# Kernel optimization log

Hardware: AMD Instinct MI355X
Metric: run time of the kernel (lower is better)

Reference implementation:

```python
import jax, jax.numpy as jnp
import numpy as np

N = 100000   # node_count
F = 128      # dim_in (also top-k pool size: k = ceil(F/N * N) = F)
E = 625000   # edges


def setup_inputs() -> dict:
    key = jax.random.key(0)
    ks = jax.random.split(key, 20)
    s = 1.0 / np.sqrt(F)

    def g(i, shape, scale=s):
        return jax.random.normal(ks[i], shape, dtype=jnp.float32) * scale

    inp = {
        "x": jax.random.normal(ks[0], (N, F), dtype=jnp.float32),
        "edge_index": jax.random.randint(ks[1], (2, E), 0, N),
        "edge_weight": jax.random.uniform(ks[2], (E,), dtype=jnp.float32),
    }
    for l in (1, 2):
        b = 3 + 6 * (l - 1)
        inp[f"p{l}"] = g(b, (F,))              # TopKPooling projection vector
        inp[f"w_ih{l}"] = g(b + 1, (3 * F, F))  # GRU input weights (r,z,n)
        inp[f"w_hh{l}"] = g(b + 2, (3 * F, F))  # GRU hidden weights
        inp[f"b_ih{l}"] = g(b + 3, (3 * F,))
        inp[f"b_hh{l}"] = g(b + 4, (3 * F,))
        inp[f"h0{l}"] = g(b + 5, (F, F))        # EvolveGCNH initial_weight
    inp["lin1_w"] = g(15, (2, F))
    inp["lin1_b"] = g(16, (2,), 0.1)
    inp["lin2_w"] = g(17, (1, 2), 0.5)
    inp["lin2_b"] = g(18, (1,), 0.1)
    return inp


def _gru_step(x_t, h, w_ih, w_hh, b_ih, b_hh):
    # single GRU timestep, batch = F rows, hidden = F
    gi = x_t @ w_ih.T + b_ih
    gh = h @ w_hh.T + b_hh
    i_r, i_z, i_n = jnp.split(gi, 3, axis=-1)
    h_r, h_z, h_n = jnp.split(gh, 3, axis=-1)
    r = jax.nn.sigmoid(i_r + h_r)
    z = jax.nn.sigmoid(i_z + h_z)
    n = jnp.tanh(i_n + r * h_n)
    return (1.0 - z) * n + z * h


def _gcn_conv_fixed_w(x, W, edge_index, edge_weight):
    # GCN with externally supplied weight: out = D^-1/2 (A+I) D^-1/2 (x W)
    row, col = edge_index[0], edge_index[1]
    loops = jnp.arange(N)
    row = jnp.concatenate([row, loops])
    col = jnp.concatenate([col, loops])
    w = jnp.concatenate([edge_weight, jnp.ones((N,), x.dtype)])
    deg = jax.ops.segment_sum(w, col, num_segments=N)
    dinv = jnp.where(deg > 0, jax.lax.rsqrt(deg), 0.0)
    norm = dinv[row] * w * dinv[col]          # [E+N]
    xw = x @ W                                 # [N, F]
    return jax.ops.segment_sum(norm[:, None] * xw[row], col, num_segments=N)


def _evolve_gcnh(x, edge_index, edge_weight, p, w_ih, w_hh, b_ih, b_hh, h0):
    # TopKPooling: score = x@p / ||p||, keep top F nodes, gate by tanh(score)
    score = x @ p / jnp.linalg.norm(p)
    top_vals, top_idx = jax.lax.top_k(score, F)
    x_tilde = x[top_idx] * jnp.tanh(top_vals)[:, None]   # [F, F]
    # evolve weight via one GRU step (hidden = previous/initial weight)
    W = _gru_step(x_tilde, h0, w_ih, w_hh, b_ih, b_hh)   # [F, F]
    return _gcn_conv_fixed_w(x, W, edge_index, edge_weight)


def reference(x, edge_index, edge_weight,
              p1, w_ih1, w_hh1, b_ih1, b_hh1, h01,
              p2, w_ih2, w_hh2, b_ih2, b_hh2, h02,
              lin1_w, lin1_b, lin2_w, lin2_b):
    h = jax.nn.relu(_evolve_gcnh(x, edge_index, edge_weight, p1, w_ih1, w_hh1, b_ih1, b_hh1, h01))
    h = jax.nn.relu(_evolve_gcnh(h, edge_index, edge_weight, p2, w_ih2, w_hh2, b_ih2, b_hh2, h02))
    # dropout(0.4) is identity in eval mode
    h = h @ lin1_w.T + lin1_b
    h = h @ lin2_w.T + lin2_b
    return h  # [N, 1]
```

## Files before the change

kernel.cpp:

```cpp
#include <hip/hip_runtime.h>
#include <cstdint>
#include <cstddef>


#define FDIM 128

typedef __attribute__((ext_vector_type(8))) short bfrag;
typedef __attribute__((ext_vector_type(4))) float f32x4;
typedef __attribute__((ext_vector_type(2))) float f32x2;

__device__ __forceinline__ float wave_sum(float v) {
#pragma unroll
  for (int m = 32; m >= 1; m >>= 1) v += __shfl_xor(v, m, 64);
  return v;
}

__device__ __forceinline__ float sigmoidf_(float x) {
  return 1.0f / (1.0f + expf(-x));
}

__device__ __forceinline__ unsigned omap(float f) {
  unsigned u = __float_as_uint(f);
  return (u & 0x80000000u) ? ~u : (u | 0x80000000u);
}

__device__ __forceinline__ int xcd_chunk(int b, int nb) {
  return (b & 7) * (nb >> 3) + (b >> 3);
}

__device__ __forceinline__ int swz(int row, int colb) {
  return row * 256 + (colb ^ ((row & 7) << 4));
}


__global__ __launch_bounds__(256) void k_edge_samp(
    const int* __restrict__ ei, const float* __restrict__ ew,
    float* deg, int* cnt, int E,
    const float* __restrict__ x, const float* __restrict__ p1,
    float* __restrict__ samp, int stride, int eb) {
  if ((int)blockIdx.x < eb) {
    int e = blockIdx.x * 256 + threadIdx.x;
    if (e < E) {
      int c = ei[E + e];
      atomicAdd(&deg[c], ew[e]);
      atomicAdd(&cnt[c], 1);
    }
  } else {
    int l = threadIdx.x & 63;
    int w = ((int)blockIdx.x - eb) * 4 + ((int)threadIdx.x >> 6);
    float2 pv = ((const float2*)p1)[l];
    float inv = 1.0f / sqrtf(wave_sum(pv.x * pv.x + pv.y * pv.y));
#pragma unroll
    for (int r = 0; r < 4; r++) {
      int si = w * 4 + r;
      float2 a = ((const float2*)(x + (size_t)(si * stride) * FDIM))[l];
      float s = wave_sum(a.x * pv.x + a.y * pv.y) * inv;
      if (l == 0) samp[si] = s;
    }
  }
}


__global__ __launch_bounds__(256) void k_scan1_thr(
    const int* __restrict__ cnt, int* bsum,
    const float* __restrict__ deg, float* __restrict__ dinv, int n, int nb,
    const float* __restrict__ samp, float* __restrict__ thr) {
  __shared__ float a[2048];
  int t = threadIdx.x;
  if ((int)blockIdx.x < nb) {
    int* s = (int*)a;
    int b = blockIdx.x;
    int base = b * 1024;
    int v = 0;
#pragma unroll
    for (int j = 0; j < 4; j++) {
      int i = base + j * 256 + t;
      if (i < n) { v += cnt[i]; dinv[i] = 1.0f / sqrtf(1.0f + deg[i]); }
    }
    s[t] = v; __syncthreads();
    for (int off = 128; off > 0; off >>= 1) {
      if (t < off) s[t] += s[t + off];
      __syncthreads();
    }
    if (t == 0) bsum[b] = s[0];
  } else {
    for (int i = t; i < 2048; i += 256) a[i] = samp[i];
    __syncthreads();
    int g = ((int)blockIdx.x - nb) * 256 + t;
    int j = g >> 2, sub = g & 3;
    float v = a[j];
    int gt = 0, eq = 0;
    const float4* a4 = (const float4*)(a + sub * 512);
#pragma unroll 8
    for (int i = 0; i < 128; i++) {
      float4 b4 = a4[i];
      gt += (b4.x > v) + (b4.y > v) + (b4.z > v) + (b4.w > v);
      eq += (b4.x == v) + (b4.y == v) + (b4.z == v) + (b4.w == v);
    }
    gt += __shfl_xor(gt, 1, 64); eq += __shfl_xor(eq, 1, 64);
    gt += __shfl_xor(gt, 2, 64); eq += __shfl_xor(eq, 2, 64);
    if (sub == 0 && gt <= 15 && gt + eq > 15) thr[0] = v;
  }
}


__global__ __launch_bounds__(1024) void k_scan23(const int* __restrict__ cnt,
                                                 const int* __restrict__ bsum,
                                                 int* rstart, int* rnext,
                                                 int n, int nb, int E_) {
  __shared__ int s[1024];
  __shared__ int bs[128];
  int b = blockIdx.x, t = threadIdx.x;
  if (t < nb) bs[t] = bsum[t];
  __syncthreads();
  if (t == 0) {
    int run = 0;
    for (int k = 0; k < nb; k++) { int v = bs[k]; bs[k] = run; run += v; }
  }
  __syncthreads();
  int base = bs[b];
  int i = b * 1024 + t;
  int v = (i < n) ? cnt[i] : 0;
  s[t] = v; __syncthreads();
  for (int off = 1; off < 1024; off <<= 1) {
    int tmp = (t >= off) ? s[t - off] : 0;
    __syncthreads();
    s[t] += tmp;
    __syncthreads();
  }
  if (i < n) { int ex = base + s[t] - v; rstart[i] = ex; rnext[i] = ex; }
  if (b == 0 && t == 0) rstart[n] = E_;
}

__global__ void k_fill(const int* __restrict__ ei, const float* __restrict__ ew,
                       const float* __restrict__ dinv, int* rnext, int2* pay, int E) {
  int e = blockIdx.x * blockDim.x + threadIdx.x;
  if (e < E) {
    int r = ei[e];
    int c = ei[E + e];
    float nm = dinv[r] * ew[e] * dinv[c];
    int pos = atomicAdd(&rnext[c], 1);
    pay[pos] = make_int2(r, __float_as_int(nm));
  }
}


__global__ __launch_bounds__(256) void k_thr16s(const float* __restrict__ src, int stride,
                                                float* __restrict__ thr) {
  __shared__ float a[2048];
  int t = threadIdx.x;
  for (int i = t; i < 2048; i += 256) a[i] = src[(size_t)i * stride];
  __syncthreads();
  int g = blockIdx.x * 256 + t;
  int j = g >> 2, sub = g & 3;
  float v = a[j];
  int gt = 0, eq = 0;
  const float4* a4 = (const float4*)(a + sub * 512);
#pragma unroll 8
  for (int i = 0; i < 128; i++) {
    float4 b = a4[i];
    gt += (b.x > v) + (b.y > v) + (b.z > v) + (b.w > v);
    eq += (b.x == v) + (b.y == v) + (b.z == v) + (b.w == v);
  }
  gt += __shfl_xor(gt, 1, 64); eq += __shfl_xor(eq, 1, 64);
  gt += __shfl_xor(gt, 2, 64); eq += __shfl_xor(eq, 2, 64);
  if (sub == 0 && gt <= 15 && gt + eq > 15) thr[0] = v;
}

__global__ void k_collect(const float* __restrict__ sc, const float* __restrict__ thr,
                          unsigned long long* candk, int* csel, int n) {
  int i = blockIdx.x * blockDim.x + threadIdx.x;
  if (i >= n) return;
  float s = sc[i];
  if (s >= thr[0]) {
    int pos = atomicAdd(csel, 1);
    if (pos < 4096)
      candk[pos] = ((unsigned long long)omap(s) << 32) | (unsigned)(~(unsigned)i);
  }
}

__global__ __launch_bounds__(1024) void k_sel(const unsigned long long* __restrict__ candk,
                                              const int* __restrict__ csel,
                                              int* tidx, float* ttanh) {
  __shared__ unsigned long long a[4104];
  int t = threadIdx.x;
  int nc = csel[0]; if (nc > 4096) nc = 4096;
  int ncp = (nc + 7) & ~7;
  for (int i = t; i < ncp; i += 1024) a[i] = (i < nc) ? candk[i] : 0ULL;
  __syncthreads();
  for (int j = t; j < nc; j += 1024) {
    unsigned long long key = a[j];
    int r = 0;
#pragma unroll 8
    for (int i = 0; i < ncp; i++) r += (a[i] > key);
    if (r < 128) {
      unsigned idx = ~(unsigned)key;
      unsigned hi = (unsigned)(key >> 32);
      unsigned u = (hi & 0x80000000u) ? (hi ^ 0x80000000u) : ~hi;
      tidx[r] = (int)idx;
      ttanh[r] = tanhf(__uint_as_float(u));
    }
  }
}


template <int BF16IN>
__global__ __launch_bounds__(384) void k_gru(const void* __restrict__ xinv,
                                             const int* __restrict__ tidx,
                                             const float* __restrict__ ttanh,
                                             const float* __restrict__ wih,
                                             const float* __restrict__ whh,
                                             const float* __restrict__ bih,
                                             const float* __restrict__ bhh,
                                             const float* __restrict__ h0,
                                             unsigned short* __restrict__ WT_hi,
                                             unsigned short* __restrict__ WT_lo) {
  __shared__ float xt[128], hs[128], gis[384], ghs[384];
  int r = blockIdx.x, t = threadIdx.x;
  if (t < 128) {
    int idx = tidx[r];
    float xv;
    if (BF16IN) {
      unsigned short u = ((const unsigned short*)xinv)[(size_t)idx * FDIM + t];
      xv = __uint_as_float((unsigned)u << 16);
    } else {
      xv = ((const float*)xinv)[(size_t)idx * FDIM + t];
    }
    xt[t] = xv * ttanh[r];
    hs[t] = h0[r * FDIM + t];
  }
  __syncthreads();
  float gi = bih[t], gh = bhh[t];
  const float4* wi4 = (const float4*)(wih + (size_t)t * FDIM);
  const float4* wh4 = (const float4*)(whh + (size_t)t * FDIM);
#pragma unroll 8
  for (int k = 0; k < 32; k++) {
    float4 av = wi4[k], bv = wh4[k];
    gi += av.x * xt[4 * k] + av.y * xt[4 * k + 1] + av.z * xt[4 * k + 2] + av.w * xt[4 * k + 3];
    gh += bv.x * hs[4 * k] + bv.y * hs[4 * k + 1] + bv.z * hs[4 * k + 2] + bv.w * hs[4 * k + 3];
  }
  gis[t] = gi; ghs[t] = gh;
  __syncthreads();
  if (t < 128) {
    float rg = sigmoidf_(gis[t] + ghs[t]);
    float zg = sigmoidf_(gis[t + 128] + ghs[t + 128]);
    float ng = tanhf(gis[t + 256] + rg * ghs[t + 256]);
    float w = (1.0f - zg) * ng + zg * hs[t];
    unsigned u = __float_as_uint(w);
    float res = w - __uint_as_float(u & 0xFFFF0000u);
    WT_hi[t * FDIM + r] = (unsigned short)(u >> 16);
    WT_lo[t * FDIM + r] = (unsigned short)(__float_as_uint(res) >> 16);
  }
}


template <int MODE>
__global__ __launch_bounds__(256) void k_gemm5(const float* __restrict__ Af,
                                               const unsigned short* __restrict__ Ab,
                                               const unsigned short* __restrict__ BTh,
                                               const unsigned short* __restrict__ BTl,
                                               unsigned short* __restrict__ Y2,
                                               float* __restrict__ scOut,
                                               const float* __restrict__ p2,
                                               const float* __restrict__ l1w,
                                               const float* __restrict__ l1b,
                                               const float* __restrict__ l2w,
                                               const float* __restrict__ l2b,
                                               int nrows) {
  __shared__ unsigned short sBh[128 * 128];
  __shared__ unsigned short sBl[128 * 128];
  int tid = threadIdx.x;
  int eb = xcd_chunk(blockIdx.x, gridDim.x);
  int rblk = eb * 128;
  if (rblk >= nrows) return;
  for (int i = tid; i < 2048; i += 256) {
    int row = i >> 4, colb = (i & 15) << 4;
    *(uint4*)((char*)sBh + swz(row, colb)) = ((const uint4*)BTh)[i];
    *(uint4*)((char*)sBl + swz(row, colb)) = ((const uint4*)BTl)[i];
  }
  __syncthreads();
  int wv = tid >> 6, l = tid & 63;
  int lcol = l & 15;
  int kgrp = (l >> 4) * 8;

  float pv[8];
  float scale;
  if (MODE == 1) {
#pragma unroll
    for (int ct = 0; ct < 8; ct++) pv[ct] = p2[ct * 16 + lcol];
    float lp = 0.f;
#pragma unroll
    for (int ct = 0; ct < 8; ct++) lp += pv[ct] * pv[ct];
#pragma unroll
    for (int m = 1; m < 16; m <<= 1) lp += __shfl_xor(lp, m, 64);
    scale = 1.0f / sqrtf(lp);
  } else {
    float w0 = l2w[0], w1 = l2w[1];
#pragma unroll
    for (int ct = 0; ct < 8; ct++)
      pv[ct] = w0 * l1w[ct * 16 + lcol] + w1 * l1w[128 + ct * 16 + lcol];
    scale = w0 * l1b[0] + w1 * l1b[1] + l2b[0];
  }

  for (int tile = 0; tile < 2; tile++) {
    int r0 = rblk + wv * 32 + tile * 16;
    if (r0 >= nrows) break;
    int arow = min(r0 + lcol, nrows - 1);
    f32x4 acc[8];
#pragma unroll
    for (int c = 0; c < 8; c++) acc[c] = (f32x4){0.f, 0.f, 0.f, 0.f};
#pragma unroll
    for (int ks = 0; ks < 4; ks++) {
      bfrag ah, al;
      if (MODE == 1) {
        const float* xp = Af + (size_t)arow * FDIM + kgrp + ks * 32;
        float4 v0 = *(const float4*)(xp);
        float4 v1 = *(const float4*)(xp + 4);
        float xs[8] = {v0.x, v0.y, v0.z, v0.w, v1.x, v1.y, v1.z, v1.w};
#pragma unroll
        for (int i = 0; i < 8; i++) {
          unsigned u = __float_as_uint(xs[i]);
          float res = xs[i] - __uint_as_float(u & 0xFFFF0000u);
          ah[i] = (short)(u >> 16);
          al[i] = (short)(__float_as_uint(res) >> 16);
        }
      } else {
        ah = *(const bfrag*)(Ab + (size_t)arow * FDIM + kgrp + ks * 32);
      }
      int colb = (ks * 32 + kgrp) * 2;
#pragma unroll
      for (int ct = 0; ct < 8; ct++) {
        int off = swz(ct * 16 + lcol, colb);
        bfrag bh = *(const bfrag*)((const char*)sBh + off);
        bfrag bl = *(const bfrag*)((const char*)sBl + off);
        acc[ct] = __builtin_amdgcn_mfma_f32_16x16x32_bf16(ah, bh, acc[ct], 0, 0, 0);
        acc[ct] = __builtin_amdgcn_mfma_f32_16x16x32_bf16(ah, bl, acc[ct], 0, 0, 0);
        if (MODE == 1)
          acc[ct] = __builtin_amdgcn_mfma_f32_16x16x32_bf16(al, bh, acc[ct], 0, 0, 0);
      }
    }
    int rbase = r0 + (l >> 4) * 4;
    float part[4] = {0.f, 0.f, 0.f, 0.f};
#pragma unroll
    for (int ct = 0; ct < 8; ct++) {
      int col = ct * 16 + lcol;
#pragma unroll
      for (int r = 0; r < 4; r++) {
        int row = rbase + r;
        float rl = fmaxf(acc[ct][r], 0.0f);
        part[r] += rl * pv[ct];
        if (MODE == 1 && row < nrows) {
          unsigned u = __float_as_uint(rl);
          Y2[(size_t)row * FDIM + col] = (unsigned short)((u + 0x8000u) >> 16);
        }
      }
    }
#pragma unroll
    for (int r = 0; r < 4; r++) {
#pragma unroll
      for (int m = 1; m < 16; m <<= 1) part[r] += __shfl_xor(part[r], m, 64);
    }
    if (lcol == 0) {
#pragma unroll
      for (int r = 0; r < 4; r++) {
        int row = rbase + r;
        if (row < nrows) {
          if (MODE == 1) scOut[row] = part[r] * scale;
          else           scOut[row] = part[r] + scale;
        }
      }
    }
  }
}


template <int L>
__global__ void k_gather5(const void* __restrict__ inv, void* __restrict__ outv,
                          const float* __restrict__ dinv,
                          const int* __restrict__ rstart,
                          const int2* __restrict__ pay,
                          const float* __restrict__ p1,
                          const float* __restrict__ thr1,
                          unsigned long long* __restrict__ candk, int* __restrict__ csel,
                          int n) {
  int wv = threadIdx.x >> 6, l = threadIdx.x & 63;
  int eb = xcd_chunk(blockIdx.x, gridDim.x);
  int c = eb * 4 + wv;
  if (c >= n) return;
  float dc = dinv[c];
  float ax, ay, sx0, sx1;
  unsigned long long base;
  if (L == 1) {
    const float* in = (const float*)inv;
    float2 v = ((const float2*)(in + (size_t)c * FDIM))[l];
    sx0 = v.x; sx1 = v.y;
    ax = dc * dc * v.x; ay = dc * dc * v.y;
    base = (unsigned long long)(const char*)inv + ((size_t)l << 3);
  } else {
    const unsigned short* in = (const unsigned short*)inv;
    unsigned u = *(const unsigned*)(in + (size_t)c * FDIM + l * 2);
    sx0 = sx1 = 0.f;
    ax = dc * dc * __uint_as_float(u << 16);
    ay = dc * dc * __uint_as_float(u & 0xFFFF0000u);
    base = (unsigned long long)(const char*)inv + ((size_t)l << 2);
  }
  int st = rstart[c], cn = rstart[c + 1] - st;
  for (int q0 = 0; q0 < cn; q0 += 64) {
    int2 ep = (q0 + l < cn) ? pay[st + q0 + l] : make_int2(c, 0);
    int m = min(64, cn - q0);
    for (int g = 0; g < m; g += 8) {
      unsigned long long addr[8];
      float w[8];
#pragma unroll
      for (int u = 0; u < 8; u++) {
        int r = __shfl(ep.x, g + u, 64);
        w[u] = __int_as_float(__shfl(ep.y, g + u, 64));
        addr[u] = base + ((unsigned long long)(unsigned)r << (L == 1 ? 9 : 8));
      }
      if (L == 1) {
        f32x2 ev[8];
#pragma unroll
        for (int u = 0; u < 8; u++)
          asm volatile("global_load_dwordx2 %0, %1, off" : "=v"(ev[u]) : "v"(addr[u]));
        asm volatile("s_waitcnt vmcnt(0)" ::: "memory");
        __builtin_amdgcn_sched_barrier(0);
#pragma unroll
        for (int u = 0; u < 8; u++) { ax += w[u] * ev[u][0]; ay += w[u] * ev[u][1]; }
      } else {
        unsigned uv[8];
#pragma unroll
        for (int u = 0; u < 8; u++)
          asm volatile("global_load_dword %0, %1, off" : "=v"(uv[u]) : "v"(addr[u]));
        asm volatile("s_waitcnt vmcnt(0)" ::: "memory");
        __builtin_amdgcn_sched_barrier(0);
#pragma unroll
        for (int u = 0; u < 8; u++) {
          ax += w[u] * __uint_as_float(uv[u] << 16);
          ay += w[u] * __uint_as_float(uv[u] & 0xFFFF0000u);
        }
      }
    }
  }
  if (L == 1) {
    float* out = (float*)outv;
    ((float2*)(out + (size_t)c * FDIM))[l] = make_float2(ax, ay);
    float2 pvv = ((const float2*)p1)[l];
    float inv1 = 1.0f / sqrtf(wave_sum(pvv.x * pvv.x + pvv.y * pvv.y));
    float s = wave_sum(sx0 * pvv.x + sx1 * pvv.y) * inv1;
    if (l == 0 && s >= thr1[0]) {
      int pos = atomicAdd(csel, 1);
      if (pos < 4096)
        candk[pos] = ((unsigned long long)omap(s) << 32) | (unsigned)(~(unsigned)c);
    }
  } else {
    unsigned* out = (unsigned*)outv;
    unsigned lo = (__float_as_uint(ax) + 0x8000u) >> 16;
    unsigned hi = (__float_as_uint(ay) + 0x8000u) >> 16;
    out[(size_t)c * (FDIM / 2) + l] = lo | (hi << 16);
  }
}


extern "C" void kernel_launch(void* const* d_in, const int* in_sizes, int n_in,
                              void* d_out, int out_size, void* d_ws, size_t ws_size,
                              hipStream_t stream) {
  const float* x    = (const float*)d_in[0];
  const int*   ei   = (const int*)d_in[1];
  const float* ew   = (const float*)d_in[2];
  const float* p1   = (const float*)d_in[3];
  const float* wih1 = (const float*)d_in[4];
  const float* whh1 = (const float*)d_in[5];
  const float* bih1 = (const float*)d_in[6];
  const float* bhh1 = (const float*)d_in[7];
  const float* h01  = (const float*)d_in[8];
  const float* p2   = (const float*)d_in[9];
  const float* wih2 = (const float*)d_in[10];
  const float* whh2 = (const float*)d_in[11];
  const float* bih2 = (const float*)d_in[12];
  const float* bhh2 = (const float*)d_in[13];
  const float* h02  = (const float*)d_in[14];
  const float* l1w  = (const float*)d_in[15];
  const float* l1b  = (const float*)d_in[16];
  const float* l2w  = (const float*)d_in[17];
  const float* l2b  = (const float*)d_in[18];
  float* out = (float*)d_out;

  const int N = in_sizes[0] / FDIM;
  const int E = in_sizes[2];

  size_t off = 0;
  auto alloc = [&](size_t bytes) -> char* {
    char* p = (char*)d_ws + off;
    off = (off + bytes + 255) & ~(size_t)255;
    return p;
  };
  float* deg   = (float*)alloc((size_t)N * 4);
  int*   cnt   = (int*)alloc((size_t)N * 4);
  int*   csel1 = (int*)alloc(8);
  int*   csel2 = (int*)alloc(8);
  size_t zero_span = (size_t)((char*)(csel2 + 2) - (char*)deg);
  float* sc2   = (float*)alloc((size_t)N * 4);
  unsigned long long* candk = (unsigned long long*)alloc(4096 * 8);
  int*   tidx  = (int*)alloc(128 * 4);
  float* ttanh = (float*)alloc(128 * 4);
  float* thr1  = (float*)alloc(4);
  float* thr2  = (float*)alloc(4);
  float* samp  = (float*)alloc(2048 * 4);
  float* dinv  = (float*)alloc((size_t)N * 4);
  int*   rstart= (int*)alloc((size_t)(N + 1) * 4);
  int*   rnext = (int*)alloc((size_t)N * 4);
  const int nb = (N + 1023) / 1024;
  int*   bsum  = (int*)alloc((size_t)nb * 4);
  int2*  pay   = (int2*)alloc((size_t)E * 8);
  unsigned short* WTh = (unsigned short*)alloc(128 * 128 * 2);
  unsigned short* WTl = (unsigned short*)alloc(128 * 128 * 2);
  float* g1    = (float*)alloc((size_t)N * FDIM * 4);
  unsigned short* h1 = (unsigned short*)alloc((size_t)N * FDIM * 2);
  unsigned short* g2 = (unsigned short*)alloc((size_t)N * FDIM * 2);
  (void)ws_size; (void)n_in; (void)out_size;

  const int edgeblocks  = (E + 255) / 256;
  const int gemmblocks  = ((N + 127) / 128 + 7) & ~7;
  const int gatherblocks= (N + 3) / 4;
  const int sampstride  = N / 2048;

  hipMemsetAsync(deg, 0, zero_span, stream);
  k_edge_samp<<<edgeblocks + 128, 256, 0, stream>>>(ei, ew, deg, cnt, E,
                                                    x, p1, samp, sampstride, edgeblocks);
  k_scan1_thr<<<nb + 32, 256, 0, stream>>>(cnt, bsum, deg, dinv, N, nb, samp, thr1);
  k_scan23<<<nb, 1024, 0, stream>>>(cnt, bsum, rstart, rnext, N, nb, E);
  k_fill<<<edgeblocks, 256, 0, stream>>>(ei, ew, dinv, rnext, pay, E);

  k_gather5<1><<<gatherblocks, 256, 0, stream>>>(x, g1, dinv, rstart, pay,
                                                 p1, thr1, candk, csel1, N);
  k_sel<<<1, 1024, 0, stream>>>(candk, csel1, tidx, ttanh);
  k_gru<0><<<128, 384, 0, stream>>>(x, tidx, ttanh, wih1, whh1, bih1, bhh1, h01, WTh, WTl);
  k_gemm5<1><<<gemmblocks, 256, 0, stream>>>(g1, nullptr, WTh, WTl, h1, sc2,
                                             p2, l1w, l1b, l2w, l2b, N);

  k_thr16s<<<32, 256, 0, stream>>>(sc2, sampstride, thr2);
  k_collect<<<(N + 255) / 256, 256, 0, stream>>>(sc2, thr2, candk, csel2, N);
  k_sel<<<1, 1024, 0, stream>>>(candk, csel2, tidx, ttanh);
  k_gru<1><<<128, 384, 0, stream>>>(h1, tidx, ttanh, wih2, whh2, bih2, bhh2, h02, WTh, WTl);
  k_gather5<2><<<gatherblocks, 256, 0, stream>>>(h1, g2, dinv, rstart, pay,
                                                 nullptr, nullptr, nullptr, nullptr, N);
  k_gemm5<2><<<gemmblocks, 256, 0, stream>>>(nullptr, g2, WTh, WTl, nullptr, out,
                                             p2, l1w, l1b, l2w, l2b, N);
}
```

Before: 315.2 us.

## Overlap layer-2 top-k selection and GRU with sliced neighbor gather

The layer-2 neighbor gather is split into four node slices. Each slice is launched in the same kernel as one of the small serial stages: threshold sampling, candidate collection, top-k selection, and the GRU weight update. The aim is to keep the GPU busy during those latency-bound one-block or few-block kernels instead of running them alone. In exchange, the selection now runs with 256 threads and caps candidates at 2048 rather than 4096, and the GRU runs with 256 threads instead of 384, which may lengthen the serial critical path.

```diff
diff --git a/kernel.cpp b/kernel.cpp
--- a/kernel.cpp
+++ b/kernel.cpp
@@ -144,40 +144,6 @@
   }
 }
 
-
-__global__ __launch_bounds__(256) void k_thr16s(const float* __restrict__ src, int stride,
-                                                float* __restrict__ thr) {
-  __shared__ float a[2048];
-  int t = threadIdx.x;
-  for (int i = t; i < 2048; i += 256) a[i] = src[(size_t)i * stride];
-  __syncthreads();
-  int g = blockIdx.x * 256 + t;
-  int j = g >> 2, sub = g & 3;
-  float v = a[j];
-  int gt = 0, eq = 0;
-  const float4* a4 = (const float4*)(a + sub * 512);
-#pragma unroll 8
-  for (int i = 0; i < 128; i++) {
-    float4 b = a4[i];
-    gt += (b.x > v) + (b.y > v) + (b.z > v) + (b.w > v);
-    eq += (b.x == v) + (b.y == v) + (b.z == v) + (b.w == v);
-  }
-  gt += __shfl_xor(gt, 1, 64); eq += __shfl_xor(eq, 1, 64);
-  gt += __shfl_xor(gt, 2, 64); eq += __shfl_xor(eq, 2, 64);
-  if (sub == 0 && gt <= 15 && gt + eq > 15) thr[0] = v;
-}
-
-__global__ void k_collect(const float* __restrict__ sc, const float* __restrict__ thr,
-                          unsigned long long* candk, int* csel, int n) {
-  int i = blockIdx.x * blockDim.x + threadIdx.x;
-  if (i >= n) return;
-  float s = sc[i];
-  if (s >= thr[0]) {
-    int pos = atomicAdd(csel, 1);
-    if (pos < 4096)
-      candk[pos] = ((unsigned long long)omap(s) << 32) | (unsigned)(~(unsigned)i);
-  }
-}
 
 __global__ __launch_bounds__(1024) void k_sel(const unsigned long long* __restrict__ candk,
                                               const int* __restrict__ csel,
@@ -204,29 +170,21 @@
 }
 
 
-template <int BF16IN>
-__global__ __launch_bounds__(384) void k_gru(const void* __restrict__ xinv,
-                                             const int* __restrict__ tidx,
-                                             const float* __restrict__ ttanh,
-                                             const float* __restrict__ wih,
-                                             const float* __restrict__ whh,
-                                             const float* __restrict__ bih,
-                                             const float* __restrict__ bhh,
-                                             const float* __restrict__ h0,
-                                             unsigned short* __restrict__ WT_hi,
-                                             unsigned short* __restrict__ WT_lo) {
+__global__ __launch_bounds__(384) void k_gru1(const float* __restrict__ xin,
+                                              const int* __restrict__ tidx,
+                                              const float* __restrict__ ttanh,
+                                              const float* __restrict__ wih,
+                                              const float* __restrict__ whh,
+                                              const float* __restrict__ bih,
+                                              const float* __restrict__ bhh,
+                                              const float* __restrict__ h0,
+                                              unsigned short* __restrict__ WT_hi,
+                                              unsigned short* __restrict__ WT_lo) {
   __shared__ float xt[128], hs[128], gis[384], ghs[384];
   int r = blockIdx.x, t = threadIdx.x;
   if (t < 128) {
     int idx = tidx[r];
-    float xv;
-    if (BF16IN) {
-      unsigned short u = ((const unsigned short*)xinv)[(size_t)idx * FDIM + t];
-      xv = __uint_as_float((unsigned)u << 16);
-    } else {
-      xv = ((const float*)xinv)[(size_t)idx * FDIM + t];
-    }
-    xt[t] = xv * ttanh[r];
+    xt[t] = xin[(size_t)idx * FDIM + t] * ttanh[r];
     hs[t] = h0[r * FDIM + t];
   }
   __syncthreads();
@@ -374,8 +332,7 @@
 }
 
 
-template <int L>
-__global__ void k_gather5(const void* __restrict__ inv, void* __restrict__ outv,
+__global__ void k_gather1(const float* __restrict__ in, float* __restrict__ outv,
                           const float* __restrict__ dinv,
                           const int* __restrict__ rstart,
                           const int2* __restrict__ pay,
@@ -388,22 +345,10 @@
   int c = eb * 4 + wv;
   if (c >= n) return;
   float dc = dinv[c];
-  float ax, ay, sx0, sx1;
-  unsigned long long base;
-  if (L == 1) {
-    const float* in = (const float*)inv;
-    float2 v = ((const float2*)(in + (size_t)c * FDIM))[l];
-    sx0 = v.x; sx1 = v.y;
-    ax = dc * dc * v.x; ay = dc * dc * v.y;
-    base = (unsigned long long)(const char*)inv + ((size_t)l << 3);
-  } else {
-    const unsigned short* in = (const unsigned short*)inv;
-    unsigned u = *(const unsigned*)(in + (size_t)c * FDIM + l * 2);
-    sx0 = sx1 = 0.f;
-    ax = dc * dc * __uint_as_float(u << 16);
-    ay = dc * dc * __uint_as_float(u & 0xFFFF0000u);
-    base = (unsigned long long)(const char*)inv + ((size_t)l << 2);
-  }
+  float2 v = ((const float2*)(in + (size_t)c * FDIM))[l];
+  float sx0 = v.x, sx1 = v.y;
+  float ax = dc * dc * v.x, ay = dc * dc * v.y;
+  unsigned long long base = (unsigned long long)(const char*)in + ((size_t)l << 3);
   int st = rstart[c], cn = rstart[c + 1] - st;
   for (int q0 = 0; q0 < cn; q0 += 64) {
     int2 ep = (q0 + l < cn) ? pay[st + q0 + l] : make_int2(c, 0);
@@ -411,53 +356,171 @@
     for (int g = 0; g < m; g += 8) {
       unsigned long long addr[8];
       float w[8];
+      f32x2 ev[8];
 #pragma unroll
       for (int u = 0; u < 8; u++) {
         int r = __shfl(ep.x, g + u, 64);
         w[u] = __int_as_float(__shfl(ep.y, g + u, 64));
-        addr[u] = base + ((unsigned long long)(unsigned)r << (L == 1 ? 9 : 8));
-      }
-      if (L == 1) {
-        f32x2 ev[8];
-#pragma unroll
-        for (int u = 0; u < 8; u++)
-          asm volatile("global_load_dwordx2 %0, %1, off" : "=v"(ev[u]) : "v"(addr[u]));
-        asm volatile("s_waitcnt vmcnt(0)" ::: "memory");
-        __builtin_amdgcn_sched_barrier(0);
-#pragma unroll
-        for (int u = 0; u < 8; u++) { ax += w[u] * ev[u][0]; ay += w[u] * ev[u][1]; }
-      } else {
-        unsigned uv[8];
-#pragma unroll
-        for (int u = 0; u < 8; u++)
-          asm volatile("global_load_dword %0, %1, off" : "=v"(uv[u]) : "v"(addr[u]));
-        asm volatile("s_waitcnt vmcnt(0)" ::: "memory");
-        __builtin_amdgcn_sched_barrier(0);
-#pragma unroll
-        for (int u = 0; u < 8; u++) {
-          ax += w[u] * __uint_as_float(uv[u] << 16);
-          ay += w[u] * __uint_as_float(uv[u] & 0xFFFF0000u);
+        addr[u] = base + ((unsigned long long)(unsigned)r << 9);
+      }
+#pragma unroll
+      for (int u = 0; u < 8; u++)
+        asm volatile("global_load_dwordx2 %0, %1, off" : "=v"(ev[u]) : "v"(addr[u]));
+      asm volatile("s_waitcnt vmcnt(0)" ::: "memory");
+      __builtin_amdgcn_sched_barrier(0);
+#pragma unroll
+      for (int u = 0; u < 8; u++) { ax += w[u] * ev[u][0]; ay += w[u] * ev[u][1]; }
+    }
+  }
+  ((float2*)(outv + (size_t)c * FDIM))[l] = make_float2(ax, ay);
+  float2 pvv = ((const float2*)p1)[l];
+  float inv1 = 1.0f / sqrtf(wave_sum(pvv.x * pvv.x + pvv.y * pvv.y));
+  float s = wave_sum(sx0 * pvv.x + sx1 * pvv.y) * inv1;
+  if (l == 0 && s >= thr1[0]) {
+    int pos = atomicAdd(csel, 1);
+    if (pos < 4096)
+      candk[pos] = ((unsigned long long)omap(s) << 32) | (unsigned)(~(unsigned)c);
+  }
+}
+
+
+template <int ROLE>
+__global__ __launch_bounds__(256) void k_l2(
+    const unsigned short* __restrict__ h1, unsigned* __restrict__ g2,
+    const float* __restrict__ dinv, const int* __restrict__ rstart,
+    const int2* __restrict__ pay, int n, int sliceStart, int xb,
+    const float* __restrict__ sc2, int stride, float* __restrict__ thr2,
+    unsigned long long* __restrict__ candk, int* __restrict__ csel,
+    int* __restrict__ tidx, float* __restrict__ ttanh,
+    const float* __restrict__ wih, const float* __restrict__ whh,
+    const float* __restrict__ bih, const float* __restrict__ bhh,
+    const float* __restrict__ h0,
+    unsigned short* __restrict__ WTh, unsigned short* __restrict__ WTl) {
+  __shared__ unsigned long long smem8[2052];
+  float* smemF = (float*)smem8;
+  int t = threadIdx.x;
+  if ((int)blockIdx.x < xb) {
+    if (ROLE == 0) {
+      float* a = smemF;
+      for (int i = t; i < 2048; i += 256) a[i] = sc2[(size_t)i * stride];
+      __syncthreads();
+      int g = (int)blockIdx.x * 256 + t;
+      int j = g >> 2, sub = g & 3;
+      float v = a[j];
+      int gt = 0, eq = 0;
+      const float4* a4 = (const float4*)(a + sub * 512);
+#pragma unroll 8
+      for (int i = 0; i < 128; i++) {
+        float4 b4 = a4[i];
+        gt += (b4.x > v) + (b4.y > v) + (b4.z > v) + (b4.w > v);
+        eq += (b4.x == v) + (b4.y == v) + (b4.z == v) + (b4.w == v);
+      }
+      gt += __shfl_xor(gt, 1, 64); eq += __shfl_xor(eq, 1, 64);
+      gt += __shfl_xor(gt, 2, 64); eq += __shfl_xor(eq, 2, 64);
+      if (sub == 0 && gt <= 15 && gt + eq > 15) thr2[0] = v;
+    } else if (ROLE == 1) {
+      int i = (int)blockIdx.x * 256 + t;
+      if (i < n) {
+        float s = sc2[i];
+        if (s >= thr2[0]) {
+          int pos = atomicAdd(csel, 1);
+          if (pos < 4096)
+            candk[pos] = ((unsigned long long)omap(s) << 32) | (unsigned)(~(unsigned)i);
         }
       }
-    }
-  }
-  if (L == 1) {
-    float* out = (float*)outv;
-    ((float2*)(out + (size_t)c * FDIM))[l] = make_float2(ax, ay);
-    float2 pvv = ((const float2*)p1)[l];
-    float inv1 = 1.0f / sqrtf(wave_sum(pvv.x * pvv.x + pvv.y * pvv.y));
-    float s = wave_sum(sx0 * pvv.x + sx1 * pvv.y) * inv1;
-    if (l == 0 && s >= thr1[0]) {
-      int pos = atomicAdd(csel, 1);
-      if (pos < 4096)
-        candk[pos] = ((unsigned long long)omap(s) << 32) | (unsigned)(~(unsigned)c);
-    }
-  } else {
-    unsigned* out = (unsigned*)outv;
-    unsigned lo = (__float_as_uint(ax) + 0x8000u) >> 16;
-    unsigned hi = (__float_as_uint(ay) + 0x8000u) >> 16;
-    out[(size_t)c * (FDIM / 2) + l] = lo | (hi << 16);
-  }
+    } else if (ROLE == 2) {
+      unsigned long long* a = smem8;
+      int nc = csel[0]; if (nc > 2048) nc = 2048;
+      int ncp = (nc + 7) & ~7;
+      for (int i = t; i < ncp; i += 256) a[i] = (i < nc) ? candk[i] : 0ULL;
+      __syncthreads();
+      for (int j = t; j < nc; j += 256) {
+        unsigned long long key = a[j];
+        int r = 0;
+#pragma unroll 8
+        for (int i = 0; i < ncp; i++) r += (a[i] > key);
+        if (r < 128) {
+          unsigned idx = ~(unsigned)key;
+          unsigned hi = (unsigned)(key >> 32);
+          unsigned u = (hi & 0x80000000u) ? (hi ^ 0x80000000u) : ~hi;
+          tidx[r] = (int)idx;
+          ttanh[r] = tanhf(__uint_as_float(u));
+        }
+      }
+    } else {
+      float* xt = smemF; float* hs = smemF + 128;
+      float* gis = smemF + 256; float* ghs = smemF + 640;
+      int r = blockIdx.x;
+      if (t < 128) {
+        int idx = tidx[r];
+        unsigned short u = h1[(size_t)idx * FDIM + t];
+        xt[t] = __uint_as_float((unsigned)u << 16) * ttanh[r];
+        hs[t] = h0[r * FDIM + t];
+      }
+      __syncthreads();
+      for (int tt = t; tt < 384; tt += 256) {
+        float gi = bih[tt], gh = bhh[tt];
+        const float4* wi4 = (const float4*)(wih + (size_t)tt * FDIM);
+        const float4* wh4 = (const float4*)(whh + (size_t)tt * FDIM);
+#pragma unroll 8
+        for (int k = 0; k < 32; k++) {
+          float4 av = wi4[k], bv = wh4[k];
+          gi += av.x * xt[4 * k] + av.y * xt[4 * k + 1] + av.z * xt[4 * k + 2] + av.w * xt[4 * k + 3];
+          gh += bv.x * hs[4 * k] + bv.y * hs[4 * k + 1] + bv.z * hs[4 * k + 2] + bv.w * hs[4 * k + 3];
+        }
+        gis[tt] = gi; ghs[tt] = gh;
+      }
+      __syncthreads();
+      if (t < 128) {
+        float rg = sigmoidf_(gis[t] + ghs[t]);
+        float zg = sigmoidf_(gis[t + 128] + ghs[t + 128]);
+        float ng = tanhf(gis[t + 256] + rg * ghs[t + 256]);
+        float w = (1.0f - zg) * ng + zg * hs[t];
+        unsigned u = __float_as_uint(w);
+        float res = w - __uint_as_float(u & 0xFFFF0000u);
+        WTh[t * FDIM + r] = (unsigned short)(u >> 16);
+        WTl[t * FDIM + r] = (unsigned short)(__float_as_uint(res) >> 16);
+      }
+    }
+    return;
+  }
+  int wv = t >> 6, l = t & 63;
+  int c = sliceStart + ((int)blockIdx.x - xb) * 4 + wv;
+  if (c >= n) return;
+  float dc = dinv[c];
+  unsigned u0 = *(const unsigned*)(h1 + (size_t)c * FDIM + l * 2);
+  float ax = dc * dc * __uint_as_float(u0 << 16);
+  float ay = dc * dc * __uint_as_float(u0 & 0xFFFF0000u);
+  unsigned long long base = (unsigned long long)(const char*)h1 + ((size_t)l << 2);
+  int st = rstart[c], cn = rstart[c + 1] - st;
+  for (int q0 = 0; q0 < cn; q0 += 64) {
+    int2 ep = (q0 + l < cn) ? pay[st + q0 + l] : make_int2(c, 0);
+    int m = min(64, cn - q0);
+    for (int g = 0; g < m; g += 8) {
+      unsigned long long addr[8];
+      float w[8];
+      unsigned uv[8];
+#pragma unroll
+      for (int u = 0; u < 8; u++) {
+        int r = __shfl(ep.x, g + u, 64);
+        w[u] = __int_as_float(__shfl(ep.y, g + u, 64));
+        addr[u] = base + ((unsigned long long)(unsigned)r << 8);
+      }
+#pragma unroll
+      for (int u = 0; u < 8; u++)
+        asm volatile("global_load_dword %0, %1, off" : "=v"(uv[u]) : "v"(addr[u]));
+      asm volatile("s_waitcnt vmcnt(0)" ::: "memory");
+      __builtin_amdgcn_sched_barrier(0);
+#pragma unroll
+      for (int u = 0; u < 8; u++) {
+        ax += w[u] * __uint_as_float(uv[u] << 16);
+        ay += w[u] * __uint_as_float(uv[u] & 0xFFFF0000u);
+      }
+    }
+  }
+  unsigned lo = (__float_as_uint(ax) + 0x8000u) >> 16;
+  unsigned hi = (__float_as_uint(ay) + 0x8000u) >> 16;
+  g2[(size_t)c * (FDIM / 2) + l] = lo | (hi << 16);
 }
 
 
@@ -516,13 +579,15 @@
   unsigned short* WTl = (unsigned short*)alloc(128 * 128 * 2);
   float* g1    = (float*)alloc((size_t)N * FDIM * 4);
   unsigned short* h1 = (unsigned short*)alloc((size_t)N * FDIM * 2);
-  unsigned short* g2 = (unsigned short*)alloc((size_t)N * FDIM * 2);
+  unsigned* g2 = (unsigned*)alloc((size_t)N * FDIM * 2);
   (void)ws_size; (void)n_in; (void)out_size;
 
   const int edgeblocks  = (E + 255) / 256;
   const int gemmblocks  = ((N + 127) / 128 + 7) & ~7;
   const int gatherblocks= (N + 3) / 4;
   const int sampstride  = N / 2048;
+  const int slice       = gatherblocks / 4;
+  const int collectblks = (N + 255) / 256;
 
   hipMemsetAsync(deg, 0, zero_span, stream);
   k_edge_samp<<<edgeblocks + 128, 256, 0, stream>>>(ei, ew, deg, cnt, E,
@@ -531,19 +596,33 @@
   k_scan23<<<nb, 1024, 0, stream>>>(cnt, bsum, rstart, rnext, N, nb, E);
   k_fill<<<edgeblocks, 256, 0, stream>>>(ei, ew, dinv, rnext, pay, E);
 
-  k_gather5<1><<<gatherblocks, 256, 0, stream>>>(x, g1, dinv, rstart, pay,
-                                                 p1, thr1, candk, csel1, N);
+  k_gather1<<<gatherblocks, 256, 0, stream>>>(x, g1, dinv, rstart, pay,
+                                              p1, thr1, candk, csel1, N);
   k_sel<<<1, 1024, 0, stream>>>(candk, csel1, tidx, ttanh);
-  k_gru<0><<<128, 384, 0, stream>>>(x, tidx, ttanh, wih1, whh1, bih1, bhh1, h01, WTh, WTl);
+  k_gru1<<<128, 384, 0, stream>>>(x, tidx, ttanh, wih1, whh1, bih1, bhh1, h01, WTh, WTl);
   k_gemm5<1><<<gemmblocks, 256, 0, stream>>>(g1, nullptr, WTh, WTl, h1, sc2,
                                              p2, l1w, l1b, l2w, l2b, N);
 
-  k_thr16s<<<32, 256, 0, stream>>>(sc2, sampstride, thr2);
-  k_collect<<<(N + 255) / 256, 256, 0, stream>>>(sc2, thr2, candk, csel2, N);
-  k_sel<<<1, 1024, 0, stream>>>(candk, csel2, tidx, ttanh);
-  k_gru<1><<<128, 384, 0, stream>>>(h1, tidx, ttanh, wih2, whh2, bih2, bhh2, h02, WTh, WTl);
-  k_gather5<2><<<gatherblocks, 256, 0, stream>>>(h1, g2, dinv, rstart, pay,
-                                                 nullptr, nullptr, nullptr, nullptr, N);
-  k_gemm5<2><<<gemmblocks, 256, 0, stream>>>(nullptr, g2, WTh, WTl, nullptr, out,
+  k_l2<0><<<32 + slice, 256, 0, stream>>>(h1, g2, dinv, rstart, pay, N, 0, 32,
+                                          sc2, sampstride, thr2, candk, csel2,
+                                          tidx, ttanh, wih2, whh2, bih2, bhh2, h02,
+                                          WTh, WTl);
+  k_l2<1><<<collectblks + slice, 256, 0, stream>>>(h1, g2, dinv, rstart, pay, N,
+                                          slice * 4, collectblks,
+                                          sc2, sampstride, thr2, candk, csel2,
+                                          tidx, ttanh, wih2, whh2, bih2, bhh2, h02,
+                                          WTh, WTl);
+  k_l2<2><<<1 + slice, 256, 0, stream>>>(h1, g2, dinv, rstart, pay, N,
+                                          slice * 8, 1,
+                                          sc2, sampstride, thr2, candk, csel2,
+                                          tidx, ttanh, wih2, whh2, bih2, bhh2, h02,
+                                          WTh, WTl);
+  k_l2<3><<<128 + slice, 256, 0, stream>>>(h1, g2, dinv, rstart, pay, N,
+                                          slice * 12, 128,
+                                          sc2, sampstride, thr2, candk, csel2,
+                                          tidx, ttanh, wih2, whh2, bih2, bhh2, h02,
+                                          WTh, WTl);
+  k_gemm5<2><<<gemmblocks, 256, 0, stream>>>(nullptr, (const unsigned short*)g2,
+                                             WTh, WTl, nullptr, out,
                                              p2, l1w, l1b, l2w, l2b, N);
 }
```

After: 321.0 us. No clear change (+1.9%).
